# Kernel tuning notes

Measured on AMD Instinct MI355X. Metric: run time of the kernel, lower is better.

## Reference

```python
import jax, jax.numpy as jnp
import numpy as np

N_NODES = 524288
N_EDGES = 2097152
B = 16384
CONCAT = 128 + 128 + 881  # 1137


def _glorot(key, shape):
    fan_in, fan_out = shape[0], shape[1]
    s = jnp.sqrt(6.0 / (fan_in + fan_out))
    return jax.random.uniform(key, shape, jnp.float32, -s, s)


def setup_inputs() -> dict:
    key = jax.random.key(0)
    ks = jax.random.split(key, 24)
    inp = {
        'drug_x': jax.random.normal(ks[0], (N_NODES, 30), jnp.float32),
        'edge_index': jax.random.randint(ks[1], (2, N_EDGES), 0, N_NODES, jnp.int32),
        'batch': jnp.sort(jax.random.randint(ks[2], (N_NODES,), 0, B, jnp.int32)),
        'protein_x': jax.random.normal(ks[3], (B, 979), jnp.float32),
        'fppubchem': jax.random.uniform(ks[4], (B, 881), jnp.float32),
        # GCN layers (PyG GCNConv: linear no-bias, bias added after aggregation)
        'W1': _glorot(ks[5], (30, 64)), 'b1': jnp.zeros((64,), jnp.float32),
        'W2': _glorot(ks[6], (64, 64)), 'b2': jnp.zeros((64,), jnp.float32),
        'W3': _glorot(ks[7], (64, 64)), 'b3': jnp.zeros((64,), jnp.float32),
        'fc_drug_w': _glorot(ks[8], (64, 128)), 'fc_drug_b': jnp.zeros((128,), jnp.float32),
        'fc_prot_w': _glorot(ks[9], (979, 128)), 'fc_prot_b': jnp.zeros((128,), jnp.float32),
        'fc1_w': _glorot(ks[10], (CONCAT, 512)), 'fc1_b': jnp.zeros((512,), jnp.float32),
        'fc2_w': _glorot(ks[11], (512, 256)), 'fc2_b': jnp.zeros((256,), jnp.float32),
        'fc3_w': _glorot(ks[12], (256, 1)), 'fc3_b': jnp.zeros((1,), jnp.float32),
    }
    return inp


def _gcn_layer(x, W, b, src, dst, deg_inv_sqrt, n_nodes):
    # x' = D^-1/2 (A+I) D^-1/2 (x W) + b   (src/dst already include self-loops)
    h = x @ W
    norm = deg_inv_sqrt[src] * deg_inv_sqrt[dst]  # [E+N]
    msg = h[src] * norm[:, None]
    out = jax.ops.segment_sum(msg, dst, num_segments=n_nodes)
    return out + b


def reference(drug_x, edge_index, batch, protein_x, fppubchem,
              W1, b1, W2, b2, W3, b3,
              fc_drug_w, fc_drug_b, fc_prot_w, fc_prot_b,
              fc1_w, fc1_b, fc2_w, fc2_b, fc3_w, fc3_b):
    n = drug_x.shape[0]
    loops = jnp.arange(n, dtype=edge_index.dtype)
    src = jnp.concatenate([edge_index[0], loops])
    dst = jnp.concatenate([edge_index[1], loops])
    deg = jax.ops.segment_sum(jnp.ones_like(src, jnp.float32), dst, num_segments=n)
    deg_inv_sqrt = jnp.where(deg > 0, jax.lax.rsqrt(jnp.maximum(deg, 1.0)), 0.0)

    h = jax.nn.relu(_gcn_layer(drug_x, W1, b1, src, dst, deg_inv_sqrt, n))
    h = jax.nn.relu(_gcn_layer(h, W2, b2, src, dst, deg_inv_sqrt, n))
    h = jax.nn.relu(_gcn_layer(h, W3, b3, src, dst, deg_inv_sqrt, n))

    # global mean pool over graphs
    nb = fppubchem.shape[0]
    sums = jax.ops.segment_sum(h, batch, num_segments=nb)
    cnts = jax.ops.segment_sum(jnp.ones((n,), jnp.float32), batch, num_segments=nb)
    pooled = sums / jnp.maximum(cnts, 1.0)[:, None]

    drug = jax.nn.relu(pooled @ fc_drug_w + fc_drug_b)
    prot = jax.nn.relu(protein_x @ fc_prot_w + fc_prot_b)
    comb = jnp.concatenate([drug, prot, fppubchem], axis=1)

    # fresh LayerNorm (weight=1, bias=0); dropout treated as identity (eval/deterministic)
    mu = jnp.mean(comb, axis=-1, keepdims=True)
    var = jnp.mean((comb - mu) ** 2, axis=-1, keepdims=True)
    comb = (comb - mu) * jax.lax.rsqrt(var + 1e-5)

    comb = jax.nn.relu(comb @ fc1_w + fc1_b)
    comb = jax.nn.relu(comb @ fc2_w + fc2_b)
    return comb @ fc3_w + fc3_b
```

## Files before the change

kernel.cpp:

```cpp
#include <hip/hip_runtime.h>
#include <hip/hip_bf16.h>

#define CONCAT_F 1137
#define CONCAT_P 1152
#define PROT_K 979
#define PROT_P 992

typedef __attribute__((ext_vector_type(8))) short bf16x8;
typedef __attribute__((ext_vector_type(4))) float f32x4;

static __device__ __forceinline__ float bfu2f(unsigned short u) {
  return __uint_as_float(((unsigned)u) << 16);
}
static __device__ __forceinline__ unsigned short f2bfu(float v) {
  __hip_bfloat16 t = __float2bfloat16(v);
  unsigned short u;
  __builtin_memcpy(&u, &t, 2);
  return u;
}

#define ACC4(A0, A1, A2, A3, U)        \
  {                                    \
    A0 += bfu2f((U).x & 0xffffu);      \
    A1 += bfu2f((U).x >> 16);          \
    A2 += bfu2f((U).y & 0xffffu);      \
    A3 += bfu2f((U).y >> 16);          \
  }

__global__ void k_count_xcd(const int* __restrict__ dst, int* __restrict__ rs,
                            int E, int shift, int chunk) {
  int cls = blockIdx.x & 7;
  int slice = blockIdx.x >> 3;
  int s0 = slice * chunk;
  int s1 = min(E, s0 + chunk);
  for (int e = s0 + threadIdx.x; e < s1; e += blockDim.x) {
    int d = dst[e];
    if ((d >> shift) == cls) atomicAdd(&rs[d], 1);
  }
}

__global__ void k_scatter_xcd(const int* __restrict__ src, const int* __restrict__ dst,
                              int* __restrict__ rs, int* __restrict__ csr,
                              int E, int shift, int chunk) {
  int cls = blockIdx.x & 7;
  int slice = blockIdx.x >> 3;
  int s0 = slice * chunk;
  int s1 = min(E, s0 + chunk);
  for (int e = s0 + threadIdx.x; e < s1; e += blockDim.x) {
    int d = dst[e];
    if ((d >> shift) == cls) {
      int pos = atomicAdd(&rs[d], 1);
      csr[pos] = src[e];
    }
  }
}

__global__ void k_scan_p1(const int* __restrict__ cnt, int* __restrict__ part,
                          float* __restrict__ dis, int n) {
  __shared__ int red[256];
  int tid = threadIdx.x;
  long base = (long)blockIdx.x * 1024 + tid * 4;
  int s = 0;
#pragma unroll
  for (int i = 0; i < 4; ++i) {
    long j = base + i;
    if (j < n) {
      int c = cnt[j];
      s += c;
      dis[j] = rsqrtf(1.0f + (float)c);
    }
  }
  red[tid] = s;
  __syncthreads();
  for (int off = 128; off; off >>= 1) {
    if (tid < off) red[tid] += red[tid + off];
    __syncthreads();
  }
  if (tid == 0) part[blockIdx.x] = red[0];
}

__global__ void k_scan_p2(int* __restrict__ part, int nb) {
  __shared__ int a[1024], b_[1024];
  int t = threadIdx.x;
  a[t] = (t < nb) ? part[t] : 0;
  __syncthreads();
  int* s = a;
  int* d = b_;
  for (int off = 1; off < 1024; off <<= 1) {
    d[t] = s[t] + ((t >= off) ? s[t - off] : 0);
    __syncthreads();
    int* tmp = s;
    s = d;
    d = tmp;
  }
  if (t < nb) part[t] = (t == 0) ? 0 : s[t - 1];
}

__global__ void k_scan_p3(int* __restrict__ rs, const int* __restrict__ part, int n) {
  __shared__ int a[256], b_[256];
  int tid = threadIdx.x;
  long base = (long)blockIdx.x * 1024 + tid * 4;
  int v[4];
#pragma unroll
  for (int i = 0; i < 4; ++i) {
    long j = base + i;
    v[i] = (j < n) ? rs[j] : 0;
  }
  a[tid] = v[0] + v[1] + v[2] + v[3];
  __syncthreads();
  int* s = a;
  int* d = b_;
  for (int off = 1; off < 256; off <<= 1) {
    d[tid] = s[tid] + ((tid >= off) ? s[tid - off] : 0);
    __syncthreads();
    int* t2 = s;
    s = d;
    d = t2;
  }
  int run = part[blockIdx.x] + ((tid == 0) ? 0 : s[tid - 1]);
#pragma unroll
  for (int i = 0; i < 4; ++i) {
    long j = base + i;
    if (j < n) {
      rs[j] = run;
      run += v[i];
    }
  }
}

template <int K, bool ACT>
__global__ __launch_bounds__(256) void k_mm(const void* __restrict__ Xv,
                                            const float* __restrict__ W,
                                            const float* __restrict__ bprev,
                                            const float* __restrict__ dis,
                                            unsigned short* __restrict__ M, int n) {
  __shared__ __align__(16) float hT[K][68];
  __shared__ __align__(16) float Ws[K * 64];
  __shared__ float disS[64];
  int tid = threadIdx.x;
  int rb = blockIdx.x * 64;
  for (int j = tid; j < K * 16; j += 256) ((float4*)Ws)[j] = ((const float4*)W)[j];
  if (tid < 64) disS[tid] = (rb + tid < n) ? dis[rb + tid] : 0.0f;
  __syncthreads();
  if constexpr (ACT) {
    const unsigned short* X = (const unsigned short*)Xv;
    int k = tid & 63;
    float bk = bprev[k];
#pragma unroll
    for (int r = tid >> 6; r < 64; r += 4) {
      float h = 0.0f;
      if (rb + r < n) {
        float raw = bfu2f(X[(long)(rb + r) * 64 + k]);
        h = fmaxf(fmaf(raw, disS[r], bk), 0.0f);
      }
      hT[k][r] = h;
    }
  } else {
    const float* X = (const float*)Xv;
    for (int idx = tid; idx < 64 * K; idx += 256) {
      int r = idx / K, k = idx - r * K;
      hT[k][r] = (rb + r < n) ? X[(long)(rb + r) * K + k] : 0.0f;
    }
  }
  __syncthreads();
  int rt = (tid & 15) * 4;
  int ct = (tid >> 4) * 4;
  float acc[4][4] = {};
#pragma unroll 5
  for (int k = 0; k < K; ++k) {
    float4 xr = *(const float4*)&hT[k][rt];
    float4 wr = *(const float4*)&Ws[k * 64 + ct];
    float xa[4] = {xr.x, xr.y, xr.z, xr.w};
    float wa[4] = {wr.x, wr.y, wr.z, wr.w};
#pragma unroll
    for (int i = 0; i < 4; ++i)
#pragma unroll
      for (int j = 0; j < 4; ++j) acc[i][j] = fmaf(xa[i], wa[j], acc[i][j]);
  }
#pragma unroll
  for (int i = 0; i < 4; ++i) {
    int row = rb + rt + i;
    if (row >= n) break;
    float dv = disS[rt + i];
    ushort4 pk;
    pk.x = f2bfu(acc[i][0] * dv);
    pk.y = f2bfu(acc[i][1] * dv);
    pk.z = f2bfu(acc[i][2] * dv);
    pk.w = f2bfu(acc[i][3] * dv);
    *(ushort4*)&M[(long)row * 64 + ct] = pk;
  }
}

static __device__ __forceinline__ void gather_rows(
    const int* __restrict__ rs, const int* __restrict__ csr,
    const unsigned short* __restrict__ Min, int node, int l16,
    float& A0, float& A1, float& A2, float& A3) {
  float a0, a1, a2, a3;
  float b0 = 0.f, b1 = 0.f, b2 = 0.f, b3 = 0.f;
  float c0 = 0.f, c1 = 0.f, c2 = 0.f, c3 = 0.f;
  float d0 = 0.f, d1 = 0.f, d2 = 0.f, d3 = 0.f;
  uint2 v = *(const uint2*)(Min + (size_t)node * 64 + l16 * 4);
  a0 = bfu2f(v.x & 0xffffu);
  a1 = bfu2f(v.x >> 16);
  a2 = bfu2f(v.y & 0xffffu);
  a3 = bfu2f(v.y >> 16);
  int start = (node == 0) ? 0 : rs[node - 1];
  int end = rs[node];
  int j = start;
  for (; j + 3 < end; j += 4) {
    int s0 = csr[j], s1 = csr[j + 1], s2 = csr[j + 2], s3 = csr[j + 3];
    uint2 u0 = *(const uint2*)(Min + (size_t)s0 * 64 + l16 * 4);
    uint2 u1 = *(const uint2*)(Min + (size_t)s1 * 64 + l16 * 4);
    uint2 u2 = *(const uint2*)(Min + (size_t)s2 * 64 + l16 * 4);
    uint2 u3 = *(const uint2*)(Min + (size_t)s3 * 64 + l16 * 4);
    ACC4(a0, a1, a2, a3, u0);
    ACC4(b0, b1, b2, b3, u1);
    ACC4(c0, c1, c2, c3, u2);
    ACC4(d0, d1, d2, d3, u3);
  }
  if (j + 1 < end) {
    int s0 = csr[j], s1 = csr[j + 1];
    uint2 u0 = *(const uint2*)(Min + (size_t)s0 * 64 + l16 * 4);
    uint2 u1 = *(const uint2*)(Min + (size_t)s1 * 64 + l16 * 4);
    ACC4(a0, a1, a2, a3, u0);
    ACC4(b0, b1, b2, b3, u1);
    j += 2;
  }
  if (j < end) {
    uint2 u0 = *(const uint2*)(Min + (size_t)csr[j] * 64 + l16 * 4);
    ACC4(a0, a1, a2, a3, u0);
  }
  A0 = (a0 + b0) + (c0 + d0);
  A1 = (a1 + b1) + (c1 + d1);
  A2 = (a2 + b2) + (c2 + d2);
  A3 = (a3 + b3) + (c3 + d3);
}

__global__ __launch_bounds__(256) void k_gmm(
    const int* __restrict__ rs, const int* __restrict__ csr,
    const unsigned short* __restrict__ Min, const float* __restrict__ dis,
    const float* __restrict__ bias, const float* __restrict__ W,
    unsigned short* __restrict__ Mout, int n) {
  __shared__ __align__(16) unsigned short As[64 * 64];
  __shared__ __align__(16) unsigned short Bt[64 * 64];
  const int tid = threadIdx.x;
  const int bm = blockIdx.x * 64;
  {
    int nn = tid & 63, k0 = (tid >> 6) * 16;
    bf16x8 v0, v1;
#pragma unroll
    for (int i = 0; i < 8; ++i) v0[i] = (short)f2bfu(W[(size_t)(k0 + i) * 64 + nn]);
#pragma unroll
    for (int i = 0; i < 8; ++i) v1[i] = (short)f2bfu(W[(size_t)(k0 + 8 + i) * 64 + nn]);
    int off0 = (nn * 128 + k0 * 2) ^ ((nn & 7) << 4);
    int off1 = (nn * 128 + (k0 + 8) * 2) ^ ((nn & 7) << 4);
    *(bf16x8*)((char*)Bt + off0) = v0;
    *(bf16x8*)((char*)Bt + off1) = v1;
  }
  const int lane = tid & 63;
  const int wv = tid >> 6;
  const int grp = lane >> 4, l16 = lane & 15;
  const float4 bb = *(const float4*)(bias + l16 * 4);
  for (int p = 0; p < 4; ++p) {
    int local = wv * 16 + p * 4 + grp;
    int node = bm + local;
    float A0 = 0.f, A1 = 0.f, A2 = 0.f, A3 = 0.f, dv = 0.f;
    if (node < n) {
      gather_rows(rs, csr, Min, node, l16, A0, A1, A2, A3);
      dv = dis[node];
    }
    ushort4 h;
    h.x = f2bfu(fmaxf(fmaf(A0, dv, bb.x), 0.f));
    h.y = f2bfu(fmaxf(fmaf(A1, dv, bb.y), 0.f));
    h.z = f2bfu(fmaxf(fmaf(A2, dv, bb.z), 0.f));
    h.w = f2bfu(fmaxf(fmaf(A3, dv, bb.w), 0.f));
    int off = (local * 128 + l16 * 8) ^ ((local & 7) << 4);
    *(ushort4*)((char*)As + off) = h;
  }
  __syncthreads();
  const int kb = lane >> 4, fr = lane & 15;
  f32x4 acc[4];
#pragma unroll
  for (int i = 0; i < 4; ++i) acc[i] = f32x4{0.f, 0.f, 0.f, 0.f};
  const int ar = wv * 16 + fr;
#pragma unroll
  for (int kc = 0; kc < 2; ++kc) {
    int aoff = (ar * 128 + kc * 64 + kb * 16) ^ ((ar & 7) << 4);
    bf16x8 a = *(const bf16x8*)((char*)As + aoff);
#pragma unroll
    for (int ni = 0; ni < 4; ++ni) {
      int nr = ni * 16 + fr;
      int boff = (nr * 128 + kc * 64 + kb * 16) ^ ((nr & 7) << 4);
      bf16x8 b = *(const bf16x8*)((char*)Bt + boff);
      acc[ni] = __builtin_amdgcn_mfma_f32_16x16x32_bf16(a, b, acc[ni], 0, 0, 0);
    }
  }
#pragma unroll
  for (int r = 0; r < 4; ++r) {
    int row = bm + wv * 16 + kb * 4 + r;
    if (row < n) {
      float dvo = dis[row];
#pragma unroll
      for (int ni = 0; ni < 4; ++ni)
        Mout[(size_t)row * 64 + ni * 16 + fr] = f2bfu(acc[ni][r] * dvo);
    }
  }
}

__global__ void k_gpool(const int* __restrict__ rs, const int* __restrict__ csr,
                        const unsigned short* __restrict__ M, const float* __restrict__ dis,
                        const float* __restrict__ b3, const int* __restrict__ batch,
                        float* __restrict__ sums, float* __restrict__ cntf, int n) {
  int w = (int)((blockIdx.x * (long)blockDim.x + threadIdx.x) >> 6);
  int lane = threadIdx.x & 63;
  int r0 = w * 8;
  if (r0 >= n) return;
  float bl = b3[lane];
  int cur = batch[r0];
  float acc = 0.f, c = 0.f;
  for (int i = 0; i < 8; ++i) {
    int node = r0 + i;
    int start = (node == 0) ? 0 : rs[node - 1];
    int end = rs[node];
    float a0 = bfu2f(M[(size_t)node * 64 + lane]);
    float a1 = 0.f, a2 = 0.f, a3 = 0.f;
    int j = start;
    for (; j + 3 < end; j += 4) {
      int s0 = csr[j], s1 = csr[j + 1], s2 = csr[j + 2], s3 = csr[j + 3];
      unsigned short u0 = M[(size_t)s0 * 64 + lane];
      unsigned short u1 = M[(size_t)s1 * 64 + lane];
      unsigned short u2 = M[(size_t)s2 * 64 + lane];
      unsigned short u3 = M[(size_t)s3 * 64 + lane];
      a0 += bfu2f(u0);
      a1 += bfu2f(u1);
      a2 += bfu2f(u2);
      a3 += bfu2f(u3);
    }
    if (j + 1 < end) {
      unsigned short u0 = M[(size_t)csr[j] * 64 + lane];
      unsigned short u1 = M[(size_t)csr[j + 1] * 64 + lane];
      a0 += bfu2f(u0);
      a1 += bfu2f(u1);
      j += 2;
    }
    if (j < end) a0 += bfu2f(M[(size_t)csr[j] * 64 + lane]);
    float h = fmaxf(fmaf((a0 + a1) + (a2 + a3), dis[node], bl), 0.f);
    int b = batch[node];
    if (b == cur) {
      acc += h;
      c += 1.f;
    } else {
      unsafeAtomicAdd(&sums[(size_t)cur * 64 + lane], acc);
      if (lane == 0) unsafeAtomicAdd(&cntf[cur], c);
      cur = b;
      acc = h;
      c = 1.f;
    }
  }
  unsafeAtomicAdd(&sums[(size_t)cur * 64 + lane], acc);
  if (lane == 0) unsafeAtomicAdd(&cntf[cur], c);
}

__global__ void k_drugfc(const float* __restrict__ sums, const float* __restrict__ cnt,
                         const float* __restrict__ W, const float* __restrict__ b,
                         float* __restrict__ out, int B) {
  __shared__ float ps[64];
  int row = blockIdx.x;
  int tid = threadIdx.x;
  float inv = 1.0f / fmaxf(cnt[row], 1.0f);
  if (tid < 64) ps[tid] = sums[(long)row * 64 + tid] * inv;
  __syncthreads();
  float acc = b[tid];
#pragma unroll 8
  for (int k = 0; k < 64; ++k) acc = fmaf(ps[k], W[k * 128 + tid], acc);
  out[(long)row * 128 + tid] = fmaxf(acc, 0.0f);
}

__global__ void k_cvt_bf16(const float* __restrict__ X, unsigned short* __restrict__ Y,
                           int Kin, int ldout) {
  int row = blockIdx.x;
  const float* xr = X + (size_t)row * Kin;
  unsigned short* yr = Y + (size_t)row * ldout;
  for (int j = threadIdx.x; j < ldout; j += 256)
    yr[j] = (j < Kin) ? f2bfu(xr[j]) : 0;
}

template <int MR, bool SPLIT, typename OT>
__global__ __launch_bounds__(256, 2) void k_gemm2(
    const unsigned short* __restrict__ A, const float* __restrict__ W,
    const float* __restrict__ bias, OT* __restrict__ C,
    int Mrows, int N, int K, int lda, int nsteps, int chunkSteps) {
  constexpr int NF = MR / 16;
  constexpr int BM = MR * 4;
  __shared__ __align__(16) unsigned short As[2][BM * 32];
  __shared__ __align__(16) unsigned short Bs[2][128 * 32];
  const int tid = threadIdx.x;
  const int lane = tid & 63;
  const int wid = tid >> 6;
  const int bm = blockIdx.x * BM;
  const int bn = blockIdx.y * 128;
  const int kb = lane >> 4, fr = lane & 15;
  const int ss0 = blockIdx.z * chunkSteps;
  const int ss1 = min(nsteps, ss0 + chunkSteps);

  f32x4 acc[NF][8];
#pragma unroll
  for (int mi = 0; mi < NF; ++mi)
#pragma unroll
    for (int j = 0; j < 8; ++j) acc[mi][j] = f32x4{0.f, 0.f, 0.f, 0.f};

  int aOff[NF];
#pragma unroll
  for (int mi = 0; mi < NF; ++mi) {
    int ar = wid * MR + mi * 16 + fr;
    aOff[mi] = (ar * 64 + kb * 16) ^ ((ar & 7) << 4);
  }
  int bOff[8];
#pragma unroll
  for (int ni = 0; ni < 8; ++ni) {
    int nr = ni * 16 + fr;
    bOff[ni] = (nr * 64 + kb * 16) ^ ((nr & 7) << 4);
  }
  int aW[NF];
  const unsigned short* aptrs[NF];
#pragma unroll
  for (int p = 0; p < NF; ++p) {
    int ch = tid + p * 256;
    int arow = ch >> 2, ac = ch & 3;
    aW[p] = (arow * 64 + ac * 16) ^ ((arow & 7) << 4);
    aptrs[p] = A + (size_t)(bm + arow) * lda + ac * 8;
  }
  const int bn_ = tid & 127, bk0 = (tid >> 7) * 2;
  int bW[2];
#pragma unroll
  for (int p = 0; p < 2; ++p) {
    int kbb = bk0 + p;
    bW[p] = (bn_ * 64 + kbb * 16) ^ ((bn_ & 7) << 4);
  }

  bf16x8 pa[NF];
  float pb[2][8];

#define LOAD_STEP(S)                                              \
  {                                                               \
    int k0 = (S) * 32;                                            \
    _Pragma("unroll") for (int p = 0; p < NF; ++p)                \
        pa[p] = *(const bf16x8*)(aptrs[p] + k0);                  \
    _Pragma("unroll") for (int p = 0; p < 2; ++p) {               \
      _Pragma("unroll") for (int i = 0; i < 8; ++i) {             \
        int gk = k0 + (bk0 + p) * 8 + i;                          \
        pb[p][i] = (gk < K) ? W[(size_t)gk * N + bn + bn_] : 0.f; \
      }                                                           \
    }                                                             \
  }
#define STORE_STEP(BUF)                                           \
  {                                                               \
    _Pragma("unroll") for (int p = 0; p < NF; ++p)                \
        *(bf16x8*)((char*)As[BUF] + aW[p]) = pa[p];               \
    _Pragma("unroll") for (int p = 0; p < 2; ++p) {               \
      bf16x8 v;                                                   \
      _Pragma("unroll") for (int i = 0; i < 8; ++i)               \
          v[i] = (short)f2bfu(pb[p][i]);                          \
      *(bf16x8*)((char*)Bs[BUF] + bW[p]) = v;                     \
    }                                                             \
  }

  LOAD_STEP(ss0);
  STORE_STEP(0);
  __syncthreads();
  int cur = 0;
  for (int s = ss0; s < ss1; ++s) {
    bool more = (s + 1 < ss1);
    if (more) LOAD_STEP(s + 1);
    bf16x8 a0[NF];
#pragma unroll
    for (int mi = 0; mi < NF; ++mi)
      a0[mi] = *(const bf16x8*)((char*)As[cur] + aOff[mi]);
#pragma unroll
    for (int ni = 0; ni < 8; ++ni) {
      bf16x8 b = *(const bf16x8*)((char*)Bs[cur] + bOff[ni]);
#pragma unroll
      for (int mi = 0; mi < NF; ++mi)
        acc[mi][ni] = __builtin_amdgcn_mfma_f32_16x16x32_bf16(a0[mi], b, acc[mi][ni], 0, 0, 0);
    }
    if (more) {
      STORE_STEP(cur ^ 1);
      __syncthreads();
      cur ^= 1;
    }
  }
  if constexpr (SPLIT) {
    float* Cz = (float*)C + (size_t)blockIdx.z * Mrows * N;
#pragma unroll
    for (int mi = 0; mi < NF; ++mi)
#pragma unroll
      for (int ni = 0; ni < 8; ++ni)
#pragma unroll
        for (int r = 0; r < 4; ++r) {
          int row = bm + wid * MR + mi * 16 + kb * 4 + r;
          int col = bn + ni * 16 + fr;
          Cz[(size_t)row * N + col] = acc[mi][ni][r];
        }
  } else {
    float bv[8];
#pragma unroll
    for (int ni = 0; ni < 8; ++ni) bv[ni] = bias[bn + ni * 16 + fr];
#pragma unroll
    for (int mi = 0; mi < NF; ++mi)
#pragma unroll
      for (int ni = 0; ni < 8; ++ni)
#pragma unroll
        for (int r = 0; r < 4; ++r) {
          int row = bm + wid * MR + mi * 16 + kb * 4 + r;
          int col = bn + ni * 16 + fr;
          float x = fmaxf(acc[mi][ni][r] + bv[ni], 0.f);
          if constexpr (__hip_internal::is_same<OT, float>::value) {
            C[(size_t)row * N + col] = x;
          } else {
            C[(size_t)row * N + col] = f2bfu(x);
          }
        }
  }
#undef LOAD_STEP
#undef STORE_STEP
}

__global__ void k_concat_ln(const float* __restrict__ drug, const float* __restrict__ protP,
                            const float* __restrict__ bp, const float* __restrict__ fpp,
                            unsigned short* __restrict__ comb, int B) {
  __shared__ float buf[CONCAT_F];
  __shared__ float rs[4], rs2[4];
  int row = blockIdx.x;
  int tid = threadIdx.x;
  const size_t MN = (size_t)B * 128;
  float s = 0.0f, s2 = 0.0f;
  for (int j = tid; j < CONCAT_F; j += 256) {
    float v;
    if (j < 128) {
      v = drug[(long)row * 128 + j];
    } else if (j < 256) {
      int c = j - 128;
      size_t o = (size_t)row * 128 + c;
      float acc = protP[o] + protP[MN + o] + protP[2 * MN + o] + protP[3 * MN + o];
      v = fmaxf(acc + bp[c], 0.0f);
    } else {
      v = fpp[(long)row * 881 + (j - 256)];
    }
    buf[j] = v;
    s += v;
    s2 += v * v;
  }
  for (int o = 32; o; o >>= 1) {
    s += __shfl_down(s, o, 64);
    s2 += __shfl_down(s2, o, 64);
  }
  int lane = tid & 63, wid = tid >> 6;
  if (lane == 0) { rs[wid] = s; rs2[wid] = s2; }
  __syncthreads();
  if (tid == 0) {
    float ts = rs[0] + rs[1] + rs[2] + rs[3];
    float ts2 = rs2[0] + rs2[1] + rs2[2] + rs2[3];
    float mu = ts / (float)CONCAT_F;
    float var = ts2 / (float)CONCAT_F - mu * mu;
    rs[0] = mu;
    rs2[0] = rsqrtf(fmaxf(var, 0.0f) + 1e-5f);
  }
  __syncthreads();
  float mu = rs[0], inv = rs2[0];
  for (int j = tid; j < CONCAT_P; j += 256) {
    unsigned short o = (j < CONCAT_F) ? f2bfu((buf[j] - mu) * inv) : 0;
    comb[(long)row * CONCAT_P + j] = o;
  }
}

__global__ void k_fc3(const float* __restrict__ X, const float* __restrict__ W,
                      const float* __restrict__ bias, float* __restrict__ out, int B) {
  int w = (int)((blockIdx.x * (long)blockDim.x + threadIdx.x) >> 6);
  int lane = threadIdx.x & 63;
  if (w >= B) return;
  float s = 0.0f;
#pragma unroll
  for (int j = 0; j < 4; ++j) s = fmaf(X[(long)w * 256 + lane + j * 64], W[lane + j * 64], s);
  for (int o = 32; o; o >>= 1) s += __shfl_down(s, o, 64);
  if (lane == 0) out[w] = s + bias[0];
}

extern "C" void kernel_launch(void* const* d_in, const int* in_sizes, int n_in,
                              void* d_out, int out_size, void* d_ws, size_t ws_size,
                              hipStream_t stream) {
  const float* drug_x = (const float*)d_in[0];
  const int* ei = (const int*)d_in[1];
  const int* batch = (const int*)d_in[2];
  const float* protein_x = (const float*)d_in[3];
  const float* fpp = (const float*)d_in[4];
  const float* W1 = (const float*)d_in[5];
  const float* b1 = (const float*)d_in[6];
  const float* W2 = (const float*)d_in[7];
  const float* b2 = (const float*)d_in[8];
  const float* W3 = (const float*)d_in[9];
  const float* b3 = (const float*)d_in[10];
  const float* Wd = (const float*)d_in[11];
  const float* bd = (const float*)d_in[12];
  const float* Wp = (const float*)d_in[13];
  const float* bp = (const float*)d_in[14];
  const float* Wf1 = (const float*)d_in[15];
  const float* bf1 = (const float*)d_in[16];
  const float* Wf2 = (const float*)d_in[17];
  const float* bf2 = (const float*)d_in[18];
  const float* Wf3 = (const float*)d_in[19];
  const float* bf3 = (const float*)d_in[20];
  float* out = (float*)d_out;

  const int N = in_sizes[0] / 30;
  const int E = in_sizes[1] / 2;
  const int B = in_sizes[4] / 881;

  int* rs = (int*)d_ws;
  float* dis = (float*)d_ws + ((size_t)N + 1);
  int* csr = (int*)d_ws + (2 * (size_t)N + 1);
  size_t oM = 2 * (size_t)N + 2 + (size_t)E;
  unsigned short* M = (unsigned short*)((float*)d_ws + oM);
  unsigned short* H = M + (size_t)N * 64;
  float* sums = (float*)d_ws + (oM + 64 * (size_t)N);
  float* cntf = sums + (size_t)B * 64;
  int* part = (int*)(cntf + B);
  unsigned short* protbh = (unsigned short*)(part + 1024);
  float* tail = (float*)d_ws;
  float* drug = tail;
  float* protP = drug + (size_t)B * 128;
  unsigned short* combh = (unsigned short*)(protP + 4 * (size_t)B * 128);
  unsigned short* act1h = combh + (size_t)B * CONCAT_P;
  float* act2 = (float*)(act1h + (size_t)B * 512);

  const int* srcIdx = ei;
  const int* dstIdx = ei + E;

  int shift = 0;
  while (((N - 1) >> shift) > 7) ++shift;
  const int CHUNK = 2048;
  int G = (E + CHUNK - 1) / CHUNK;

  k_cvt_bf16<<<B, 256, 0, stream>>>(protein_x, protbh, PROT_K, PROT_P);

  hipMemsetAsync(rs, 0, ((size_t)N + 1) * sizeof(int), stream);
  k_count_xcd<<<8 * G, 256, 0, stream>>>(dstIdx, rs, E, shift, CHUNK);
  int NB = (N + 1023) / 1024;
  k_scan_p1<<<NB, 256, 0, stream>>>(rs, part, dis, N);
  k_scan_p2<<<1, 1024, 0, stream>>>(part, NB);
  k_scan_p3<<<NB, 256, 0, stream>>>(rs, part, N);
  k_scatter_xcd<<<8 * G, 256, 0, stream>>>(srcIdx, dstIdx, rs, csr, E, shift, CHUNK);

  int mmBlocks = (N + 63) / 64;
  k_mm<30, false><<<mmBlocks, 256, 0, stream>>>(drug_x, W1, nullptr, dis, M, N);
  k_gmm<<<mmBlocks, 256, 0, stream>>>(rs, csr, M, dis, b1, W2, H, N);
  k_gmm<<<mmBlocks, 256, 0, stream>>>(rs, csr, H, dis, b2, W3, M, N);

  hipMemsetAsync(sums, 0, ((size_t)B * 64 + B) * sizeof(float), stream);
  int poolWaves = (N + 7) / 8;
  k_gpool<<<(poolWaves + 3) / 4, 256, 0, stream>>>(rs, csr, M, dis, b3, batch, sums, cntf, N);

  k_drugfc<<<B, 128, 0, stream>>>(sums, cntf, Wd, bd, drug, B);
  k_gemm2<16, true, float><<<dim3(B / 64, 1, 4), 256, 0, stream>>>(
      protbh, Wp, nullptr, protP, B, 128, PROT_K, PROT_P, 31, 8);
  k_concat_ln<<<B, 256, 0, stream>>>(drug, protP, bp, fpp, combh, B);
  k_gemm2<32, false, unsigned short><<<dim3(B / 128, 4, 1), 256, 0, stream>>>(
      combh, Wf1, bf1, act1h, B, 512, CONCAT_F, CONCAT_P, 36, 36);
  k_gemm2<16, false, float><<<dim3(B / 64, 2, 1), 256, 0, stream>>>(
      act1h, Wf2, bf2, act2, B, 256, 512, 512, 16, 16);
  k_fc3<<<(B + 3) / 4, 256, 0, stream>>>(act2, Wf3, bf3, out, B);
}
```

Before: 785.7 us.

## Restructure graph pooling to gather 4 features per lane via shared-memory staging

The final GCN aggregation plus mean-pool kernel now has each wave handle 32 nodes. Four 16-lane groups each gather 8 nodes with a shared gather_rows helper, so every lane loads four features at once instead of one. Aggregated, biased and ReLU'd rows are staged in shared memory, then each wave walks them sequentially to do the segmented pooling with atomics. This is meant to cut the many narrow 2-byte gathers and reduce atomic traffic, at the cost of shared memory use and a block barrier.

After: 801.4 us. Within noise of the previous version (+2.0%).

```diff
diff --git a/kernel.cpp b/kernel.cpp
--- a/kernel.cpp
+++ b/kernel.cpp
@@ -307,45 +307,44 @@
   }
 }
 
-__global__ void k_gpool(const int* __restrict__ rs, const int* __restrict__ csr,
-                        const unsigned short* __restrict__ M, const float* __restrict__ dis,
-                        const float* __restrict__ b3, const int* __restrict__ batch,
-                        float* __restrict__ sums, float* __restrict__ cntf, int n) {
-  int w = (int)((blockIdx.x * (long)blockDim.x + threadIdx.x) >> 6);
-  int lane = threadIdx.x & 63;
-  int r0 = w * 8;
-  if (r0 >= n) return;
-  float bl = b3[lane];
-  int cur = batch[r0];
+__global__ __launch_bounds__(256) void k_gpool(
+    const int* __restrict__ rs, const int* __restrict__ csr,
+    const unsigned short* __restrict__ M, const float* __restrict__ dis,
+    const float* __restrict__ b3, const int* __restrict__ batch,
+    float* __restrict__ sums, float* __restrict__ cntf, int n) {
+  __shared__ __align__(16) float hb[4][32][64];
+  const int tid = threadIdx.x;
+  const int wv = tid >> 6;
+  const int lane = tid & 63;
+  const int grp = lane >> 4, l16 = lane & 15;
+  long w32 = ((long)blockIdx.x * 4 + wv) * 32;
+  const bool active = w32 < n;
+  if (active) {
+    const float4 bb = *(const float4*)(b3 + l16 * 4);
+    for (int i = 0; i < 8; ++i) {
+      int local = grp * 8 + i;
+      long node = w32 + local;
+      float4 h = {0.f, 0.f, 0.f, 0.f};
+      if (node < n) {
+        float A0, A1, A2, A3;
+        gather_rows(rs, csr, M, (int)node, l16, A0, A1, A2, A3);
+        float dv = dis[node];
+        h.x = fmaxf(fmaf(A0, dv, bb.x), 0.f);
+        h.y = fmaxf(fmaf(A1, dv, bb.y), 0.f);
+        h.z = fmaxf(fmaf(A2, dv, bb.z), 0.f);
+        h.w = fmaxf(fmaf(A3, dv, bb.w), 0.f);
+      }
+      *(float4*)&hb[wv][local][l16 * 4] = h;
+    }
+  }
+  __syncthreads();
+  if (!active) return;
+  int last = (int)((n - w32 < 32) ? (n - w32) : 32);
+  int cur = batch[w32];
   float acc = 0.f, c = 0.f;
-  for (int i = 0; i < 8; ++i) {
-    int node = r0 + i;
-    int start = (node == 0) ? 0 : rs[node - 1];
-    int end = rs[node];
-    float a0 = bfu2f(M[(size_t)node * 64 + lane]);
-    float a1 = 0.f, a2 = 0.f, a3 = 0.f;
-    int j = start;
-    for (; j + 3 < end; j += 4) {
-      int s0 = csr[j], s1 = csr[j + 1], s2 = csr[j + 2], s3 = csr[j + 3];
-      unsigned short u0 = M[(size_t)s0 * 64 + lane];
-      unsigned short u1 = M[(size_t)s1 * 64 + lane];
-      unsigned short u2 = M[(size_t)s2 * 64 + lane];
-      unsigned short u3 = M[(size_t)s3 * 64 + lane];
-      a0 += bfu2f(u0);
-      a1 += bfu2f(u1);
-      a2 += bfu2f(u2);
-      a3 += bfu2f(u3);
-    }
-    if (j + 1 < end) {
-      unsigned short u0 = M[(size_t)csr[j] * 64 + lane];
-      unsigned short u1 = M[(size_t)csr[j + 1] * 64 + lane];
-      a0 += bfu2f(u0);
-      a1 += bfu2f(u1);
-      j += 2;
-    }
-    if (j < end) a0 += bfu2f(M[(size_t)csr[j] * 64 + lane]);
-    float h = fmaxf(fmaf((a0 + a1) + (a2 + a3), dis[node], bl), 0.f);
-    int b = batch[node];
+  for (int i = 0; i < last; ++i) {
+    float h = hb[wv][i][lane];
+    int b = batch[w32 + i];
     if (b == cur) {
       acc += h;
       c += 1.f;
@@ -656,7 +655,7 @@
   k_gmm<<<mmBlocks, 256, 0, stream>>>(rs, csr, H, dis, b2, W3, M, N);
 
   hipMemsetAsync(sums, 0, ((size_t)B * 64 + B) * sizeof(float), stream);
-  int poolWaves = (N + 7) / 8;
+  int poolWaves = (N + 31) / 32;
   k_gpool<<<(poolWaves + 3) / 4, 256, 0, stream>>>(rs, csr, M, dis, b3, batch, sums, cntf, N);
 
   k_drugfc<<<B, 128, 0, stream>>>(sums, cntf, Wd, bd, drug, B);
```
